# Performance work log

Hardware: AMD Instinct MI355X
Metric: run time of the kernel (lower is better)

Reference implementation:

```python
import jax, jax.numpy as jnp
import numpy as np

B, S, D = 4, 2048, 1024
H, DH = 16, 64  # dim_q = dim_k = D // H
DFF = 4096


def setup_inputs() -> dict:
    key = jax.random.key(0)
    ks = jax.random.split(key, 12)
    sd = 0.02
    x = jax.random.normal(ks[0], (B, S, D), dtype=jnp.float32)
    mask = jax.random.randint(ks[1], (B, S, S), 0, 2) == 1  # True = masked
    Wq = jax.random.normal(ks[2], (H, D, DH), dtype=jnp.float32) * sd
    bq = jnp.zeros((H, DH), dtype=jnp.float32)
    Wk = jax.random.normal(ks[3], (H, D, DH), dtype=jnp.float32) * sd
    bk = jnp.zeros((H, DH), dtype=jnp.float32)
    Wv = jax.random.normal(ks[4], (H, D, DH), dtype=jnp.float32) * sd
    bv = jnp.zeros((H, DH), dtype=jnp.float32)
    Wo = jax.random.normal(ks[5], (H * DH, D), dtype=jnp.float32) * sd
    bo = jnp.zeros((D,), dtype=jnp.float32)
    W1 = jax.random.normal(ks[6], (D, DFF), dtype=jnp.float32) * sd
    b1 = jnp.zeros((DFF,), dtype=jnp.float32)
    W2 = jax.random.normal(ks[7], (DFF, D), dtype=jnp.float32) * sd
    b2 = jnp.zeros((D,), dtype=jnp.float32)
    return dict(x=x, mask=mask, Wq=Wq, bq=bq, Wk=Wk, bk=bk, Wv=Wv, bv=bv,
                Wo=Wo, bo=bo, W1=W1, b1=b1, W2=W2, b2=b2)


def reference(x, mask, Wq, bq, Wk, bk, Wv, bv, Wo, bo, W1, b1, W2, b2):
    # x: [B,S,D]; mask: [B,S,S] bool (True -> masked)
    # Per-head projections, batched over heads: [B,H,S,DH]
    q = jnp.einsum('bsd,hde->bhse', x, Wq) + bq[None, :, None, :]
    k = jnp.einsum('bsd,hde->bhse', x, Wk) + bk[None, :, None, :]
    v = jnp.einsum('bsd,hde->bhse', x, Wv) + bv[None, :, None, :]
    # NOTE: source scales by sqrt(seq_len) (query.size(1)), reproduced faithfully.
    scale = x.shape[1] ** 0.5
    scores = jnp.einsum('bhse,bhte->bhst', q, k) / scale  # [B,H,S,S]
    scores = jnp.where(mask[:, None, :, :], -1e9, scores)
    attn = jax.nn.softmax(scores, axis=-1)
    ctx = jnp.einsum('bhst,bhte->bhse', attn, v)  # [B,H,S,DH]
    # concat heads -> [B,S,H*DH], output projection
    ctx = jnp.transpose(ctx, (0, 2, 1, 3)).reshape(x.shape[0], x.shape[1], -1)
    out = ctx @ Wo + bo
    # FFN (no residual/LayerNorm in source; dropout = identity in eval)
    h = jax.nn.relu(out @ W1 + b1)
    return h @ W2 + b2
```

## Files before the change

### kernel.cpp

```cpp
#include <hip/hip_runtime.h>
#include <hip/hip_bf16.h>


#define SDIM 2048
#define DDIM 1024

using floatx4 = __attribute__((ext_vector_type(4))) float;
using bf16x8  = __attribute__((ext_vector_type(8))) __bf16;
using bf16x4  = __attribute__((ext_vector_type(4))) __bf16;
using short4v = __attribute__((ext_vector_type(4))) short;

#define GLDS16(gptr, lptr)                                                        \
    __builtin_amdgcn_global_load_lds(                                             \
        (const __attribute__((address_space(1))) void*)(uintptr_t)(gptr),         \
        (__attribute__((address_space(3))) void*)(uintptr_t)(lptr), 16, 0, 0)


__global__ void k_f2b(const float* __restrict__ in, __bf16* __restrict__ out) {
    long i = ((long)blockIdx.x * 256 + threadIdx.x) * 4;
    float4 f = *(const float4*)(in + i);
    bf16x4 v;
    v[0] = (__bf16)f.x; v[1] = (__bf16)f.y; v[2] = (__bf16)f.z; v[3] = (__bf16)f.w;
    *(bf16x4*)(out + i) = v;
}

__global__ void k_tr(const float* __restrict__ in, __bf16* __restrict__ out, int R, int C) {
    __shared__ float t[32][33];
    int nrt = R >> 5;
    int tr = blockIdx.x % nrt, tc = blockIdx.x / nrt;
    int r0 = tr * 32, c0 = tc * 32;
    int lx = threadIdx.x & 31, ly = threadIdx.x >> 5;
    #pragma unroll
    for (int i = 0; i < 32; i += 8) t[ly + i][lx] = in[(long)(r0 + ly + i) * C + c0 + lx];
    __syncthreads();
    #pragma unroll
    for (int i = 0; i < 32; i += 8) out[(long)(c0 + ly + i) * R + r0 + lx] = (__bf16)t[lx][ly + i];
}

__global__ void k_pack_qkvw(const float* __restrict__ Wq, const float* __restrict__ Wk,
                            const float* __restrict__ Wv, __bf16* __restrict__ out) {
    int bid = blockIdx.x;
    int dht = bid & 1;
    int dt = (bid >> 1) & 31;
    int h = (bid >> 6) & 15;
    int which = bid >> 10;
    const float* W = (which == 0) ? Wq : (which == 1) ? Wk : Wv;
    __shared__ float t[32][33];
    int lx = threadIdx.x & 31, ly = threadIdx.x >> 5;
    const float* src = W + ((long)h * 1024 + dt * 32) * 64 + dht * 32;
    #pragma unroll
    for (int i = 0; i < 32; i += 8) t[ly + i][lx] = src[(ly + i) * 64 + lx];
    __syncthreads();
    __bf16* dst = out + ((long)(which * 1024 + h * 64 + dht * 32)) * 1024 + dt * 32;
    #pragma unroll
    for (int i = 0; i < 32; i += 8) dst[(long)(ly + i) * 1024 + lx] = (__bf16)t[lx][ly + i];
}

__global__ void k_pack_qkvb(const float* bq, const float* bk, const float* bv, float* out) {
    int i = blockIdx.x * 256 + threadIdx.x;
    if (i < 3072) {
        int which = i >> 10, r = i & 1023;
        const float* s = (which == 0) ? bq : (which == 1) ? bk : bv;
        out[i] = s[r];
    }
}

__global__ void k_probe(const unsigned* __restrict__ m, int* flag) {
    __shared__ int bad;
    if (threadIdx.x == 0) bad = 0;
    __syncthreads();
    int local = 0;
    for (int i = 0; i < 64; i++) {
        unsigned w = m[threadIdx.x + 256 * i];
        if (w != 0u && w != 1u && w != 0x3f800000u) local = 1;
    }
    if (local) atomicOr(&bad, 1);
    __syncthreads();
    if (threadIdx.x == 0) *flag = bad ? 0 : 1;
}

__global__ void k_pack_mask(const void* __restrict__ mask, const int* __restrict__ flag,
                            unsigned long long* __restrict__ bits) {
    long wid = ((long)blockIdx.x * 256 + threadIdx.x) >> 6;
    int lane = threadIdx.x & 63;
    long e = wid * 64 + lane;
    bool pred;
    if (*flag) pred = ((const unsigned*)mask)[e] != 0u;
    else       pred = ((const unsigned char*)mask)[e] != 0;
    unsigned long long bal = __ballot(pred);
    if (lane == 0) bits[wid] = bal;
}

__global__ void k_trv(const __bf16* __restrict__ Vrow, __bf16* __restrict__ Vt) {
    __shared__ __bf16 t[32][72];
    int p = blockIdx.x >> 6, ts = blockIdx.x & 63;
    int tid = threadIdx.x;
    const __bf16* src = Vrow + ((long)p * 2048 + ts * 32) * 64;
    int s = tid >> 3, c = (tid & 7) * 8;
    *(bf16x8*)&t[s][c] = *(const bf16x8*)&src[s * 64 + c];
    __syncthreads();
    int dh = tid >> 2, sb = (tid & 3) * 8;
    bf16x8 w;
    #pragma unroll
    for (int j = 0; j < 8; j++) w[j] = t[sb + j][dh];
    *(bf16x8*)&Vt[((long)p * 64 + dh) * 2048 + ts * 32 + sb] = w;
}

#define QSZ 8388608L

template <int MODE>
__global__ __launch_bounds__(256, 3) void k_gemm(const __bf16* __restrict__ A,
                                                 const __bf16* __restrict__ Bt,
                                                 const float* __restrict__ bias,
                                                 void* __restrict__ Cout, int Ndim, int K) {
    __shared__ __align__(16) __bf16 As[128 * 64];
    __shared__ __align__(16) __bf16 Bs[128 * 64];
    const int tid = threadIdx.x;
    const int wave = tid >> 6, lane = tid & 63;
    const int q = lane >> 4, l16 = lane & 15;
    const int wr = wave >> 1, wc = wave & 1;
    const long bm = (long)blockIdx.x * 128;
    const long bn = (long)blockIdx.y * 128;
    floatx4 acc[4][4] = {};

    const int srow = lane >> 3;
    const int scol = (((lane & 7) - srow) & 7) * 8;
    const int r8 = l16 & 7;

    for (int k0 = 0; k0 < K; k0 += 64) {
        __syncthreads();
        #pragma unroll
        for (int c = 0; c < 4; c++) {
            int row0 = wave * 32 + c * 8;
            GLDS16(&A[(bm + row0 + srow) * K + k0 + scol], (char*)As + row0 * 128);
            GLDS16(&Bt[(bn + row0 + srow) * K + k0 + scol], (char*)Bs + row0 * 128);
        }
        __syncthreads();
        #pragma unroll
        for (int s = 0; s < 2; s++) {
            bf16x8 af[4], bfr[4];
            #pragma unroll
            for (int i = 0; i < 4; i++)
                af[i] = *(const bf16x8*)&As[(wr * 64 + i * 16 + l16) * 64 + ((s * 4 + q + r8) & 7) * 8];
            #pragma unroll
            for (int j = 0; j < 4; j++)
                bfr[j] = *(const bf16x8*)&Bs[(wc * 64 + j * 16 + l16) * 64 + ((s * 4 + q + r8) & 7) * 8];
            #pragma unroll
            for (int i = 0; i < 4; i++)
                #pragma unroll
                for (int j = 0; j < 4; j++)
                    acc[i][j] = __builtin_amdgcn_mfma_f32_16x16x32_bf16(af[i], bfr[j], acc[i][j], 0, 0, 0);
        }
    }

    const int mrow0 = (int)bm + wr * 64 + q * 4;
    const int ncol0 = (int)bn + wc * 64;
    #pragma unroll
    for (int j = 0; j < 4; j++) {
        int nbase = ncol0 + j * 16 + l16;
        float bv = bias[nbase];
        #pragma unroll
        for (int i = 0; i < 4; i++) {
            #pragma unroll
            for (int r = 0; r < 4; r++) {
                int mm = mrow0 + i * 16 + r;
                float v = acc[i][j][r] + bv;
                if (MODE == 2) v = fmaxf(v, 0.f);
                if (MODE == 3) {
                    ((float*)Cout)[(long)mm * Ndim + nbase] = v;
                } else if (MODE == 0) {
                    int which = nbase >> 10, rem = nbase & 1023;
                    int hh = rem >> 6, dh = rem & 63;
                    int bb = mm >> 11, ss = mm & 2047;
                    long pr = (long)(bb * 16 + hh);
                    __bf16* o = (__bf16*)Cout;
                    if (which == 0) {
                        v *= 0.03188152837f;
                        o[(pr * 2048 + ss) * 64 + dh] = (__bf16)v;
                    } else if (which == 1) o[QSZ + (pr * 2048 + ss) * 64 + dh] = (__bf16)v;
                    else o[3 * QSZ + (pr * 2048 + ss) * 64 + dh] = (__bf16)v;
                } else {
                    ((__bf16*)Cout)[(long)mm * Ndim + nbase] = (__bf16)v;
                }
            }
        }
    }
}

__global__ __launch_bounds__(256, 4) void k_attn(const __bf16* __restrict__ Q,
                                                 const __bf16* __restrict__ Kb,
                                                 const __bf16* __restrict__ Vt,
                                                 const unsigned* __restrict__ bitw,
                                                 __bf16* __restrict__ ctx) {
    __shared__ __align__(16) __bf16 Qs[64 * 64];
    __shared__ __align__(16) __bf16 Ks[128 * 64];
    __shared__ __align__(16) __bf16 Vts[64 * 128];
    const int tid = threadIdx.x, wave = tid >> 6, lane = tid & 63;
    const int q = lane >> 4, l16 = lane & 15;
    const int pair = blockIdx.x & 63, qt = blockIdx.x >> 6;
    const int b = pair >> 4, h = pair & 15;

    const int srow8 = lane >> 3;
    const int scol8 = (((lane & 7) - srow8) & 7) * 8;
    const int r8 = l16 & 7;
    const int vrow = lane >> 4;
    const int vl = lane & 15;

    const __bf16* Qp = Q + ((long)pair * SDIM + qt * 64) * 64;
    #pragma unroll
    for (int c = 0; c < 2; c++) {
        int row0 = wave * 16 + c * 8;
        GLDS16(&Qp[(row0 + srow8) * 64 + scol8], (char*)Qs + row0 * 128);
    }
    __syncthreads();
    const bf16x8 qf0 = *(const bf16x8*)&Qs[(wave * 16 + l16) * 64 + ((q + r8) & 7) * 8];
    const bf16x8 qf1 = *(const bf16x8*)&Qs[(wave * 16 + l16) * 64 + ((q + 4 + r8) & 7) * 8];

    float lacc = 0.f;
    floatx4 o[4] = {};
    const long mrow0 = (long)b * SDIM + qt * 64;

    for (int kt = 0; kt < 16; kt++) {
        __syncthreads();
        const __bf16* Kp = Kb + ((long)pair * SDIM + kt * 128) * 64;
        #pragma unroll
        for (int c = 0; c < 4; c++) {
            int row0 = wave * 32 + c * 8;
            GLDS16(&Kp[(row0 + srow8) * 64 + scol8], (char*)Ks + row0 * 128);
        }
        const __bf16* Vp = Vt + ((long)pair * 64) * SDIM + kt * 128;
        #pragma unroll
        for (int c = 0; c < 4; c++) {
            int row0 = wave * 16 + c * 4;
            int gsrc = ((vl - (c * 4 + vrow)) & 15) * 8;
            GLDS16(&Vp[(long)(row0 + vrow) * SDIM + gsrc], (char*)Vts + row0 * 256);
        }
        const uint4 mq = *(const uint4*)(bitw + ((mrow0 + wave * 16 + l16) << 6) + kt * 4);
        __syncthreads();

        floatx4 st[8];
        #pragma unroll
        for (int ct = 0; ct < 8; ct++) {
            bf16x8 kf0 = *(const bf16x8*)&Ks[(ct * 16 + l16) * 64 + ((q + r8) & 7) * 8];
            bf16x8 kf1 = *(const bf16x8*)&Ks[(ct * 16 + l16) * 64 + ((q + 4 + r8) & 7) * 8];
            floatx4 z = {};
            z = __builtin_amdgcn_mfma_f32_16x16x32_bf16(kf0, qf0, z, 0, 0, 0);
            z = __builtin_amdgcn_mfma_f32_16x16x32_bf16(kf1, qf1, z, 0, 0, 0);
            st[ct] = z;
        }
        unsigned mwv[4] = {mq.x, mq.y, mq.z, mq.w};
        #pragma unroll
        for (int ct = 0; ct < 8; ct++) {
            unsigned wd = mwv[ct >> 1];
            int bp = ((ct & 1) << 4) + q * 4;
            #pragma unroll
            for (int r = 0; r < 4; r++) {
                float p = exp2f(st[ct][r]);
                p = ((wd >> (bp + r)) & 1u) ? 0.f : p;
                st[ct][r] = p;
                lacc += p;
            }
        }
        #pragma unroll
        for (int ct = 0; ct < 8; ct++) {
            union { bf16x4 b; short4v s; } pu;
            #pragma unroll
            for (int r = 0; r < 4; r++) pu.b[r] = (__bf16)st[ct][r];
            #pragma unroll
            for (int d = 0; d < 4; d++) {
                int vg = (ct * 2 + (q >> 1) + l16) & 15;
                union { bf16x4 b; short4v s; } vu;
                vu.b = *(const bf16x4*)((const char*)Vts + (d * 16 + l16) * 256 + vg * 16 + (q & 1) * 8);
                o[d] = __builtin_amdgcn_mfma_f32_16x16x16bf16_1k(vu.s, pu.s, o[d], 0, 0, 0);
            }
        }
    }
    lacc += __shfl_xor(lacc, 16);
    lacc += __shfl_xor(lacc, 32);
    float inv = 1.0f / lacc;
    int rowg = qt * 64 + wave * 16 + l16;
    long base = ((long)b * SDIM + rowg) * DDIM + h * 64;
    #pragma unroll
    for (int d = 0; d < 4; d++) {
        bf16x4 w;
        #pragma unroll
        for (int r = 0; r < 4; r++) w[r] = (__bf16)(o[d][r] * inv);
        *(bf16x4*)&ctx[base + d * 16 + q * 4] = w;
    }
}


extern "C" void kernel_launch(void* const* d_in, const int* in_sizes, int n_in,
                              void* d_out, int out_size, void* d_ws, size_t ws_size,
                              hipStream_t stream) {
    const float* x = (const float*)d_in[0];
    const void* mask = d_in[1];
    const float* Wq = (const float*)d_in[2];
    const float* bq = (const float*)d_in[3];
    const float* Wk = (const float*)d_in[4];
    const float* bk = (const float*)d_in[5];
    const float* Wv = (const float*)d_in[6];
    const float* bv = (const float*)d_in[7];
    const float* Wo = (const float*)d_in[8];
    const float* bo = (const float*)d_in[9];
    const float* W1 = (const float*)d_in[10];
    const float* b1 = (const float*)d_in[11];
    const float* W2 = (const float*)d_in[12];
    const float* b2 = (const float*)d_in[13];

    char* ws = (char*)d_ws;
    __bf16* xb   = (__bf16*)(ws + 0);
    __bf16* Qb   = (__bf16*)(ws + 16777216);
    __bf16* Kb   = (__bf16*)(ws + 33554432);
    __bf16* Vtb  = (__bf16*)(ws + 50331648);
    __bf16* Vrow = (__bf16*)(ws + 67108864);
    __bf16* hbuf = (__bf16*)(ws + 33554432);
    __bf16* wqkvt = (__bf16*)(ws + 100663296);
    __bf16* wot  = (__bf16*)(ws + 106954752);
    __bf16* w1t  = (__bf16*)(ws + 109051904);
    __bf16* w2t  = (__bf16*)(ws + 117440512);
    float* bqkv  = (float*)(ws + 125829120);
    int* flag    = (int*)(ws + 125841408);
    __bf16* ctx = xb;
    __bf16* attn_out = Qb;
    unsigned long long* bits = (unsigned long long*)wqkvt;
    (void)Vrow;

    k_f2b<<<8192, 256, 0, stream>>>(x, xb);
    k_pack_qkvw<<<3072, 256, 0, stream>>>(Wq, Wk, Wv, wqkvt);
    k_pack_qkvb<<<12, 256, 0, stream>>>(bq, bk, bv, bqkv);
    k_tr<<<1024, 256, 0, stream>>>(Wo, wot, 1024, 1024);
    k_tr<<<4096, 256, 0, stream>>>(W1, w1t, 1024, 4096);
    k_tr<<<4096, 256, 0, stream>>>(W2, w2t, 4096, 1024);
    k_probe<<<1, 256, 0, stream>>>((const unsigned*)mask, flag);

    {
        dim3 g(64, 24);
        k_gemm<0><<<g, 256, 0, stream>>>(xb, wqkvt, bqkv, (void*)Qb, 3072, 1024);
    }
    k_trv<<<4096, 256, 0, stream>>>(Vrow, Vtb);
    k_pack_mask<<<65536, 256, 0, stream>>>(mask, flag, bits);
    k_attn<<<2048, 256, 0, stream>>>(Qb, Kb, Vtb, (const unsigned*)bits, ctx);
    {
        dim3 g(64, 8);
        k_gemm<1><<<g, 256, 0, stream>>>(ctx, wot, bo, (void*)attn_out, 1024, 1024);
    }
    {
        dim3 g(64, 32);
        k_gemm<2><<<g, 256, 0, stream>>>(attn_out, w1t, b1, (void*)hbuf, 4096, 1024);
    }
    {
        dim3 g(64, 8);
        k_gemm<3><<<g, 256, 0, stream>>>(hbuf, w2t, b2, d_out, 1024, 4096);
    }
}
```

Before: 634.8 us.

## Remap mask bits per lane, compute softmax row sums via MFMA, hoist LDS addresses

A new kernel re-packs the mask bitmap so each attention lane loads one 32-bit word per key tile instead of a uint4 and shifting per element. The attention kernel drops the per-lane row-sum accumulation and cross-lane shuffles and gets the sum from an extra MFMA against a ones vector. It also uses raw exp2 and byte-permute truncation for the bf16 conversion, and precomputes LDS pointers. The GEMM gets precomputed LDS pointers and launch bounds raised to 4 blocks, which may tighten registers. These changes trade an extra small kernel launch and slightly different rounding (truncation instead of round-to-nearest) for less per-element ALU work in the attention loop.

```diff
diff --git a/kernel.cpp b/kernel.cpp
--- a/kernel.cpp
+++ b/kernel.cpp
@@ -91,6 +91,20 @@
     if (lane == 0) bits[wid] = bal;
 }
 
+__global__ void k_remap(const unsigned* __restrict__ bitsDW, unsigned* __restrict__ out) {
+    int t = blockIdx.x * 256 + threadIdx.x;
+    int q = t & 3, kt = (t >> 2) & 15, srow = t >> 6;
+    uint4 md = *(const uint4*)(bitsDW + (long)srow * 64 + kt * 4);
+    unsigned d[4] = {md.x, md.y, md.z, md.w};
+    unsigned acc = 0;
+    #pragma unroll
+    for (int ct = 0; ct < 8; ct++) {
+        unsigned nib = (d[ct >> 1] >> (((ct & 1) << 4) + q * 4)) & 0xFu;
+        acc |= nib << (ct * 4);
+    }
+    out[t] = acc;
+}
+
 __global__ void k_trv(const __bf16* __restrict__ Vrow, __bf16* __restrict__ Vt) {
     __shared__ __bf16 t[32][72];
     int p = blockIdx.x >> 6, ts = blockIdx.x & 63;
@@ -109,7 +123,7 @@
 #define QSZ 8388608L
 
 template <int MODE>
-__global__ __launch_bounds__(256, 3) void k_gemm(const __bf16* __restrict__ A,
+__global__ __launch_bounds__(256, 4) void k_gemm(const __bf16* __restrict__ A,
                                                  const __bf16* __restrict__ Bt,
                                                  const float* __restrict__ bias,
                                                  void* __restrict__ Cout, int Ndim, int K) {
@@ -127,6 +141,11 @@
     const int scol = (((lane & 7) - srow) & 7) * 8;
     const int r8 = l16 & 7;
 
+    const char* apA0 = (const char*)As + (wr * 64 + l16) * 128 + ((q + r8) & 7) * 16;
+    const char* apA1 = (const char*)As + (wr * 64 + l16) * 128 + ((q + 4 + r8) & 7) * 16;
+    const char* apB0 = (const char*)Bs + (wc * 64 + l16) * 128 + ((q + r8) & 7) * 16;
+    const char* apB1 = (const char*)Bs + (wc * 64 + l16) * 128 + ((q + 4 + r8) & 7) * 16;
+
     for (int k0 = 0; k0 < K; k0 += 64) {
         __syncthreads();
         #pragma unroll
@@ -136,21 +155,25 @@
             GLDS16(&Bt[(bn + row0 + srow) * K + k0 + scol], (char*)Bs + row0 * 128);
         }
         __syncthreads();
-        #pragma unroll
-        for (int s = 0; s < 2; s++) {
-            bf16x8 af[4], bfr[4];
-            #pragma unroll
-            for (int i = 0; i < 4; i++)
-                af[i] = *(const bf16x8*)&As[(wr * 64 + i * 16 + l16) * 64 + ((s * 4 + q + r8) & 7) * 8];
+        bf16x8 af[4], bfr[4];
+        #pragma unroll
+        for (int i = 0; i < 4; i++) af[i] = *(const bf16x8*)(apA0 + i * 2048);
+        #pragma unroll
+        for (int j = 0; j < 4; j++) bfr[j] = *(const bf16x8*)(apB0 + j * 2048);
+        #pragma unroll
+        for (int i = 0; i < 4; i++)
             #pragma unroll
             for (int j = 0; j < 4; j++)
-                bfr[j] = *(const bf16x8*)&Bs[(wc * 64 + j * 16 + l16) * 64 + ((s * 4 + q + r8) & 7) * 8];
+                acc[i][j] = __builtin_amdgcn_mfma_f32_16x16x32_bf16(af[i], bfr[j], acc[i][j], 0, 0, 0);
+        #pragma unroll
+        for (int i = 0; i < 4; i++) af[i] = *(const bf16x8*)(apA1 + i * 2048);
+        #pragma unroll
+        for (int j = 0; j < 4; j++) bfr[j] = *(const bf16x8*)(apB1 + j * 2048);
+        #pragma unroll
+        for (int i = 0; i < 4; i++)
             #pragma unroll
-            for (int i = 0; i < 4; i++)
-                #pragma unroll
-                for (int j = 0; j < 4; j++)
-                    acc[i][j] = __builtin_amdgcn_mfma_f32_16x16x32_bf16(af[i], bfr[j], acc[i][j], 0, 0, 0);
-        }
+            for (int j = 0; j < 4; j++)
+                acc[i][j] = __builtin_amdgcn_mfma_f32_16x16x32_bf16(af[i], bfr[j], acc[i][j], 0, 0, 0);
     }
 
     const int mrow0 = (int)bm + wr * 64 + q * 4;
@@ -190,7 +213,7 @@
 __global__ __launch_bounds__(256, 4) void k_attn(const __bf16* __restrict__ Q,
                                                  const __bf16* __restrict__ Kb,
                                                  const __bf16* __restrict__ Vt,
-                                                 const unsigned* __restrict__ bitw,
+                                                 const unsigned* __restrict__ bitw2,
                                                  __bf16* __restrict__ ctx) {
     __shared__ __align__(16) __bf16 Qs[64 * 64];
     __shared__ __align__(16) __bf16 Ks[128 * 64];
@@ -213,12 +236,23 @@
         GLDS16(&Qp[(row0 + srow8) * 64 + scol8], (char*)Qs + row0 * 128);
     }
     __syncthreads();
-    const bf16x8 qf0 = *(const bf16x8*)&Qs[(wave * 16 + l16) * 64 + ((q + r8) & 7) * 8];
-    const bf16x8 qf1 = *(const bf16x8*)&Qs[(wave * 16 + l16) * 64 + ((q + 4 + r8) & 7) * 8];
-
-    float lacc = 0.f;
+    const bf16x8 qf0 = *(const bf16x8*)((const char*)Qs + (wave * 16 + l16) * 128 + ((q + r8) & 7) * 16);
+    const bf16x8 qf1 = *(const bf16x8*)((const char*)Qs + (wave * 16 + l16) * 128 + ((q + 4 + r8) & 7) * 16);
+
+    const char* kp0 = (const char*)Ks + l16 * 128 + ((q + r8) & 7) * 16;
+    const char* kp1 = (const char*)Ks + l16 * 128 + ((q + 4 + r8) & 7) * 16;
+    const char* vp[8];
+    #pragma unroll
+    for (int ct = 0; ct < 8; ct++)
+        vp[ct] = (const char*)Vts + l16 * 256 + (q & 1) * 8 + ((ct * 2 + (q >> 1) + l16) & 15) * 16;
+    const int qrow = qt * 64 + wave * 16 + l16;
+    const unsigned* mp = bitw2 + ((long)(b * SDIM + qrow)) * 64 + q;
+
     floatx4 o[4] = {};
-    const long mrow0 = (long)b * SDIM + qt * 64;
+    floatx4 o5 = {};
+    union { unsigned u; short4v s4; float f; } tmp;
+    short4v ones;
+    { union { unsigned u[2]; short4v s; } c; c.u[0] = 0x3F803F80u; c.u[1] = 0x3F803F80u; ones = c.s; }
 
     for (int kt = 0; kt < 16; kt++) {
         __syncthreads();
@@ -235,51 +269,45 @@
             int gsrc = ((vl - (c * 4 + vrow)) & 15) * 8;
             GLDS16(&Vp[(long)(row0 + vrow) * SDIM + gsrc], (char*)Vts + row0 * 256);
         }
-        const uint4 mq = *(const uint4*)(bitw + ((mrow0 + wave * 16 + l16) << 6) + kt * 4);
+        const unsigned w32 = mp[kt * 4];
         __syncthreads();
 
         floatx4 st[8];
         #pragma unroll
         for (int ct = 0; ct < 8; ct++) {
-            bf16x8 kf0 = *(const bf16x8*)&Ks[(ct * 16 + l16) * 64 + ((q + r8) & 7) * 8];
-            bf16x8 kf1 = *(const bf16x8*)&Ks[(ct * 16 + l16) * 64 + ((q + 4 + r8) & 7) * 8];
+            bf16x8 kf0 = *(const bf16x8*)(kp0 + ct * 2048);
+            bf16x8 kf1 = *(const bf16x8*)(kp1 + ct * 2048);
             floatx4 z = {};
             z = __builtin_amdgcn_mfma_f32_16x16x32_bf16(kf0, qf0, z, 0, 0, 0);
             z = __builtin_amdgcn_mfma_f32_16x16x32_bf16(kf1, qf1, z, 0, 0, 0);
             st[ct] = z;
         }
-        unsigned mwv[4] = {mq.x, mq.y, mq.z, mq.w};
         #pragma unroll
         for (int ct = 0; ct < 8; ct++) {
-            unsigned wd = mwv[ct >> 1];
-            int bp = ((ct & 1) << 4) + q * 4;
-            #pragma unroll
-            for (int r = 0; r < 4; r++) {
-                float p = exp2f(st[ct][r]);
-                p = ((wd >> (bp + r)) & 1u) ? 0.f : p;
-                st[ct][r] = p;
-                lacc += p;
-            }
-        }
-        #pragma unroll
-        for (int ct = 0; ct < 8; ct++) {
-            union { bf16x4 b; short4v s; } pu;
-            #pragma unroll
-            for (int r = 0; r < 4; r++) pu.b[r] = (__bf16)st[ct][r];
+            float p0 = __builtin_amdgcn_exp2f(st[ct][0]);
+            float p1 = __builtin_amdgcn_exp2f(st[ct][1]);
+            float p2 = __builtin_amdgcn_exp2f(st[ct][2]);
+            float p3 = __builtin_amdgcn_exp2f(st[ct][3]);
+            p0 = (w32 & (1u << (ct * 4 + 0))) ? 0.f : p0;
+            p1 = (w32 & (1u << (ct * 4 + 1))) ? 0.f : p1;
+            p2 = (w32 & (1u << (ct * 4 + 2))) ? 0.f : p2;
+            p3 = (w32 & (1u << (ct * 4 + 3))) ? 0.f : p3;
+            union { float f; unsigned u; } c0, c1, c2, c3;
+            c0.f = p0; c1.f = p1; c2.f = p2; c3.f = p3;
+            union { unsigned u[2]; short4v s; } pu;
+            pu.u[0] = __builtin_amdgcn_perm(c1.u, c0.u, 0x07060302u);
+            pu.u[1] = __builtin_amdgcn_perm(c3.u, c2.u, 0x07060302u);
             #pragma unroll
             for (int d = 0; d < 4; d++) {
-                int vg = (ct * 2 + (q >> 1) + l16) & 15;
                 union { bf16x4 b; short4v s; } vu;
-                vu.b = *(const bf16x4*)((const char*)Vts + (d * 16 + l16) * 256 + vg * 16 + (q & 1) * 8);
+                vu.b = *(const bf16x4*)(vp[ct] + d * 4096);
                 o[d] = __builtin_amdgcn_mfma_f32_16x16x16bf16_1k(vu.s, pu.s, o[d], 0, 0, 0);
             }
-        }
-    }
-    lacc += __shfl_xor(lacc, 16);
-    lacc += __shfl_xor(lacc, 32);
-    float inv = 1.0f / lacc;
-    int rowg = qt * 64 + wave * 16 + l16;
-    long base = ((long)b * SDIM + rowg) * DDIM + h * 64;
+            o5 = __builtin_amdgcn_mfma_f32_16x16x16bf16_1k(ones, pu.s, o5, 0, 0, 0);
+        }
+    }
+    float inv = 1.0f / o5[0];
+    long base = ((long)b * SDIM + qrow) * DDIM + h * 64;
     #pragma unroll
     for (int d = 0; d < 4; d++) {
         bf16x4 w;
@@ -324,6 +352,7 @@
     __bf16* ctx = xb;
     __bf16* attn_out = Qb;
     unsigned long long* bits = (unsigned long long*)wqkvt;
+    unsigned* bits2 = (unsigned*)((char*)wqkvt + 2097152);
     (void)Vrow;
 
     k_f2b<<<8192, 256, 0, stream>>>(x, xb);
@@ -340,7 +369,8 @@
     }
     k_trv<<<4096, 256, 0, stream>>>(Vrow, Vtb);
     k_pack_mask<<<65536, 256, 0, stream>>>(mask, flag, bits);
-    k_attn<<<2048, 256, 0, stream>>>(Qb, Kb, Vtb, (const unsigned*)bits, ctx);
+    k_remap<<<2048, 256, 0, stream>>>((const unsigned*)bits, bits2);
+    k_attn<<<2048, 256, 0, stream>>>(Qb, Kb, Vtb, bits2, ctx);
     {
         dim3 g(64, 8);
         k_gemm<1><<<g, 256, 0, stream>>>(ctx, wot, bo, (void*)attn_out, 1024, 1024);
```

New measurement: 584.9 us. -7.9%, faster.
